# Performance work log

Hardware: AMD Instinct MI355X
Metric: run time of the kernel (lower is better)

## Reference

```python
import jax, jax.numpy as jnp
import numpy as np

B, T, D = 2, 2048, 1024
H = 16
HD = D // H  # 64

def setup_inputs() -> dict:
    key = jax.random.key(0)
    k1, k2, k3 = jax.random.split(key, 3)
    x = jax.random.normal(k1, (B, T, D), dtype=jnp.float32)
    # Linear weights stored as [in, out] for x @ W (torch stores [out, in])
    W_qkv = jax.random.normal(k2, (D, 3 * D), dtype=jnp.float32) * (1.0 / np.sqrt(D))
    W_proj = jax.random.normal(k3, (D, D), dtype=jnp.float32) * (1.0 / np.sqrt(D))
    return {"x": x, "W_qkv": W_qkv, "W_proj": W_proj}

def reference(x, W_qkv, W_proj):
    Bx, Tx, C = x.shape
    qkv = x @ W_qkv                             # [B, T, 3D]
    q, k, v = jnp.split(qkv, 3, axis=-1)        # each [B, T, D]
    # [B, T, H, HD] -> [B, H, T, HD]
    q = q.reshape(Bx, Tx, H, HD).transpose(0, 2, 1, 3)
    k = k.reshape(Bx, Tx, H, HD).transpose(0, 2, 1, 3)
    v = v.reshape(Bx, Tx, H, HD).transpose(0, 2, 1, 3)
    scale = 1.0 / np.sqrt(HD).astype(np.float32)
    att = jnp.einsum('bhqd,bhkd->bhqk', q, k) * scale  # [B, H, T, T]
    causal = jnp.tril(jnp.ones((Tx, Tx), dtype=bool))
    att = jnp.where(causal[None, None, :, :], att, -jnp.inf)
    att = jax.nn.softmax(att, axis=-1)
    y = jnp.einsum('bhqk,bhkd->bhqd', att, v)   # [B, H, T, HD]
    y = y.transpose(0, 2, 1, 3).reshape(Bx, Tx, C)
    return y @ W_proj
```

## Files before the change

kernel.cpp:

```cpp
#include <hip/hip_runtime.h>

typedef __bf16 bf16x8 __attribute__((ext_vector_type(8)));
typedef __bf16 bf16x4 __attribute__((ext_vector_type(4)));
typedef float f32x4 __attribute__((ext_vector_type(4)));
typedef unsigned short u16;
typedef unsigned int u32;
typedef u32 u32x4 __attribute__((ext_vector_type(4)));

__device__ __forceinline__ u16 f2bf(float f) {
  u32 u = __builtin_bit_cast(u32, f);
  u += 0x7fffu + ((u >> 16) & 1u);
  return (u16)(u >> 16);
}

__device__ __forceinline__ u32 cvt_pk_bf16(float lo, float hi) {
  u32 r;
  asm("v_cvt_pk_bf16_f32 %0, %1, %2" : "=v"(r) : "v"(lo), "v"(hi));
  return r;
}

__device__ __forceinline__ float ex2(float x) {
  float r;
  asm("v_exp_f32 %0, %1" : "=v"(r) : "v"(x));
  return r;
}

__device__ __forceinline__ void gl_lds16(const u16* g, u16* l) {
  __builtin_amdgcn_global_load_lds(
      (const __attribute__((address_space(1))) u32*)g,
      (__attribute__((address_space(3))) u32*)l, 16, 0, 0);
}

__device__ __forceinline__ bf16x4 tr16(const u16* p) {
  bf16x4 r;
  auto lp = (const __attribute__((address_space(3))) u16*)p;
  asm volatile("ds_read_b64_tr_b16 %0, %1" : "=&v"(r) : "v"(lp));
  return r;
}

__global__ __launch_bounds__(256) void k_cast(const float* __restrict__ in,
                                              u16* __restrict__ out, int n8) {
  int i = blockIdx.x * 256 + threadIdx.x;
  if (i >= n8) return;
  const float4* p = (const float4*)in + (size_t)i * 2;
  float4 a = p[0], b = p[1];
  u16 r[8] = {f2bf(a.x), f2bf(a.y), f2bf(a.z), f2bf(a.w),
              f2bf(b.x), f2bf(b.y), f2bf(b.z), f2bf(b.w)};
  ((uint4*)out)[i] = *(const uint4*)r;
}

__global__ __launch_bounds__(256) void k_tcast(const float* __restrict__ in,
                                               u16* __restrict__ out, int K, int N) {
  __shared__ float tile[32][33];
  int n0 = blockIdx.x * 32, k0 = blockIdx.y * 32;
  int c = threadIdx.x & 31, r0 = (threadIdx.x >> 5) * 4;
#pragma unroll
  for (int rr = 0; rr < 4; ++rr) {
    int r = r0 + rr;
    tile[r][c] = in[(size_t)(k0 + r) * N + n0 + c];
  }
  __syncthreads();
#pragma unroll
  for (int rr = 0; rr < 4; ++rr) {
    int r = r0 + rr;
    out[(size_t)(n0 + r) * K + k0 + c] = f2bf(tile[c][r]);
  }
}

template <int EPI>
__global__ __launch_bounds__(256) void k_gemm(const u16* __restrict__ A,
                                              const u16* __restrict__ Bt,
                                              u16* __restrict__ Qp, u16* __restrict__ Kp,
                                              u16* __restrict__ Vp, float* __restrict__ Cf,
                                              int K) {
  __shared__ char smem[128 * 136 * 2];
  u16* As = (u16*)smem;
  u16* Bs = (u16*)(smem + 32768 / 2 * 2);
  Bs = (u16*)(smem + 16384);
  u16* Cs = (u16*)smem;
  const int tid = threadIdx.x;
  const int lane = tid & 63, wave = tid >> 6;
  const int l15 = lane & 15, l4 = lane >> 4;
  const int wr = wave >> 1, wc = wave & 1;
  const int tm = blockIdx.y, tn = blockIdx.x;

  int srow[4], scol[4];
#pragma unroll
  for (int i = 0; i < 4; ++i) {
    srow[i] = wave * 32 + i * 8 + (lane >> 3);
    scol[i] = ((lane & 7) ^ (srow[i] & 7)) * 8;
  }

  const f32x4 fz = {0.f, 0.f, 0.f, 0.f};
  f32x4 acc[4][4];
#pragma unroll
  for (int a = 0; a < 4; ++a)
#pragma unroll
    for (int b = 0; b < 4; ++b) acc[a][b] = fz;

  const int nk = K >> 6;
  for (int kt = 0; kt < nk; ++kt) {
#pragma unroll
    for (int i = 0; i < 4; ++i)
      gl_lds16(A + (size_t)(tm * 128 + srow[i]) * K + kt * 64 + scol[i],
               &As[(wave * 4 + i) * 512]);
#pragma unroll
    for (int i = 0; i < 4; ++i)
      gl_lds16(Bt + (size_t)(tn * 128 + srow[i]) * K + kt * 64 + scol[i],
               &Bs[(wave * 4 + i) * 512]);
    __syncthreads();
    bf16x8 af[2][4], bfr[2][4];
#pragma unroll
    for (int s = 0; s < 2; ++s) {
#pragma unroll
      for (int mi = 0; mi < 4; ++mi) {
        int row = wr * 64 + mi * 16 + l15;
        int pch = (s * 4 + l4) ^ (row & 7);
        af[s][mi] = *(const bf16x8*)&As[row * 64 + pch * 8];
      }
#pragma unroll
      for (int ni = 0; ni < 4; ++ni) {
        int row = wc * 64 + ni * 16 + l15;
        int pch = (s * 4 + l4) ^ (row & 7);
        bfr[s][ni] = *(const bf16x8*)&Bs[row * 64 + pch * 8];
      }
    }
    __builtin_amdgcn_s_setprio(1);
#pragma unroll
    for (int s = 0; s < 2; ++s)
#pragma unroll
      for (int mi = 0; mi < 4; ++mi)
#pragma unroll
        for (int ni = 0; ni < 4; ++ni)
          acc[mi][ni] = __builtin_amdgcn_mfma_f32_16x16x32_bf16(af[s][mi], bfr[s][ni],
                                                                acc[mi][ni], 0, 0, 0);
    __builtin_amdgcn_s_setprio(0);
    __syncthreads();
  }

  if (EPI == 0) {
#pragma unroll
    for (int ni = 0; ni < 4; ++ni) {
      int colb = wc * 64 + ni * 16;
      float scl = ((tn * 128 + colb) >> 10) == 0 ? 0.180336880f : 1.0f;
#pragma unroll
      for (int mi = 0; mi < 4; ++mi)
#pragma unroll
        for (int r = 0; r < 4; ++r) {
          int rowb = wr * 64 + mi * 16 + l4 * 4 + r;
          Cs[rowb * 136 + colb + l15] = f2bf(acc[mi][ni][r] * scl);
        }
    }
    __syncthreads();
#pragma unroll
    for (int pass = 0; pass < 8; ++pass) {
      int rowb = pass * 16 + (tid >> 4);
      int colb = (tid & 15) * 8;
      uint4 v = *(const uint4*)&Cs[rowb * 136 + colb];
      int rowg = tm * 128 + rowb;
      int b = rowg >> 11, t = rowg & 2047;
      int gcol = tn * 128 + colb;
      int which = gcol >> 10;
      int d = gcol & 1023;
      int h = d >> 6, hd = d & 63;
      u16* dst = which == 0 ? Qp : (which == 1 ? Kp : Vp);
      *(uint4*)&dst[(size_t)(((b * 16 + h) * 2048 + t) * 64 + hd)] = v;
    }
  } else {
    const int rbase = tm * 128 + wr * 64 + l4 * 4;
    const int cbase = tn * 128 + wc * 64 + l15;
#pragma unroll
    for (int mi = 0; mi < 4; ++mi)
#pragma unroll
      for (int r = 0; r < 4; ++r) {
        int rowg = rbase + mi * 16 + r;
#pragma unroll
        for (int ni = 0; ni < 4; ++ni)
          Cf[(size_t)rowg * 1024 + cbase + ni * 16] = acc[mi][ni][r];
      }
  }
}

__global__ __launch_bounds__(256) void k_attn(const u16* __restrict__ Q,
                                              const u16* __restrict__ K,
                                              const u16* __restrict__ V,
                                              u16* __restrict__ Y) {
  __shared__ u16 Kl[4][64 * 64];
  __shared__ u16 Vtr[4][64 * 64];
  const int tid = threadIdx.x, lane = tid & 63, wave = tid >> 6;
  const int l15 = lane & 15, l4 = lane >> 4;
  const int bh = blockIdx.y;
  const int pp = (blockIdx.x + ((blockIdx.y >> 4) << 3)) & 15;
  const int qtA = 31 - pp, qtB = pp;
  const u16* Qb = Q + (size_t)bh * 2048 * 64;
  const u16* Kb = K + (size_t)bh * 2048 * 64;
  const u16* Vb = V + (size_t)bh * 2048 * 64;
  const int b = bh >> 4, h = bh & 15;
  const f32x4 fz = {0.f, 0.f, 0.f, 0.f};

  const int kk0 = wave * 16 + (lane >> 3);
  const int kk1 = kk0 + 8;
  const int lcol0 = ((lane & 7) ^ (kk0 & 7)) * 8;
  const int lcol1 = ((lane & 7) ^ (kk1 & 7)) * 8;
  int vk[2], vhd[2];
#pragma unroll
  for (int i = 0; i < 2; ++i) {
    int o = (wave * 2 + i) * 512 + lane * 8;
    vk[i] = ((o >> 6) & 15) * 4 + ((o >> 4) & 3);
    vhd[i] = ((o >> 10) << 4) + (o & 8);
  }

  auto stage = [&](int buf, int kt) {
    gl_lds16(Kb + (size_t)(kt * 64 + kk0) * 64 + lcol0, &Kl[buf][(wave * 2 + 0) * 512]);
    gl_lds16(Kb + (size_t)(kt * 64 + kk1) * 64 + lcol1, &Kl[buf][(wave * 2 + 1) * 512]);
    gl_lds16(Vb + (size_t)(kt * 64 + vk[0]) * 64 + vhd[0], &Vtr[buf][(wave * 2 + 0) * 512]);
    gl_lds16(Vb + (size_t)(kt * 64 + vk[1]) * 64 + vhd[1], &Vtr[buf][(wave * 2 + 1) * 512]);
  };

  bf16x8 qfA[2], qfB[2];
  {
    int qrA = qtA * 64 + wave * 16 + l15;
    int qrB = qtB * 64 + wave * 16 + l15;
    qfA[0] = *(const bf16x8*)&Qb[(size_t)qrA * 64 + l4 * 8];
    qfA[1] = *(const bf16x8*)&Qb[(size_t)qrA * 64 + 32 + l4 * 8];
    qfB[0] = *(const bf16x8*)&Qb[(size_t)qrB * 64 + l4 * 8];
    qfB[1] = *(const bf16x8*)&Qb[(size_t)qrB * 64 + 32 + l4 * 8];
  }
  f32x4 oA[4] = {fz, fz, fz, fz}, oB[4] = {fz, fz, fz, fz};
  float mA = -1e30f, lsA = 0.f, mB = -1e30f, lsB = 0.f;

  stage(0, 0);
  stage(1, 1);
  stage(2, 2);

  int cur = 0, kt = 0;

#pragma unroll 1
  for (; kt <= qtB; ++kt) {
    asm volatile("s_waitcnt vmcnt(8)" ::: "memory");
    __builtin_amdgcn_s_barrier();
    __builtin_amdgcn_sched_barrier(0);

    f32x4 sA[4] = {fz, fz, fz, fz}, sB[4] = {fz, fz, fz, fz};
    __builtin_amdgcn_s_setprio(1);
#pragma unroll
    for (int s = 0; s < 2; ++s)
#pragma unroll
      for (int nb = 0; nb < 4; ++nb) {
        int kk = nb * 16 + l15;
        int ch = (s * 4 + l4) ^ (kk & 7);
        bf16x8 kf = *(const bf16x8*)&Kl[cur][kk * 64 + ch * 8];
        sA[nb] = __builtin_amdgcn_mfma_f32_16x16x32_bf16(kf, qfA[s], sA[nb], 0, 0, 0);
        sB[nb] = __builtin_amdgcn_mfma_f32_16x16x32_bf16(kf, qfB[s], sB[nb], 0, 0, 0);
      }
    __builtin_amdgcn_s_setprio(0);

    float vA[16], vB[16];
#pragma unroll
    for (int nb = 0; nb < 4; ++nb)
#pragma unroll
      for (int r = 0; r < 4; ++r) {
        vA[nb * 4 + r] = sA[nb][r];
        vB[nb * 4 + r] = sB[nb][r];
      }
    if (kt == qtB) {
      int qg = wave * 16 + l15;
#pragma unroll
      for (int i = 0; i < 16; ++i) {
        int kg = (i >> 2) * 16 + l4 * 4 + (i & 3);
        if (kg > qg) vB[i] = -1e30f;
      }
    }
    float tA[8], tB[8];
#pragma unroll
    for (int i = 0; i < 8; ++i) {
      tA[i] = fmaxf(vA[2 * i], vA[2 * i + 1]);
      tB[i] = fmaxf(vB[2 * i], vB[2 * i + 1]);
    }
#pragma unroll
    for (int i = 0; i < 4; ++i) {
      tA[i] = fmaxf(tA[i], tA[i + 4]);
      tB[i] = fmaxf(tB[i], tB[i + 4]);
    }
    float mxA = fmaxf(fmaxf(tA[0], tA[2]), fmaxf(tA[1], tA[3]));
    float mxB = fmaxf(fmaxf(tB[0], tB[2]), fmaxf(tB[1], tB[3]));
    if (!__all(fmaxf(mxA - mA, mxB - mB) <= 8.0f)) {
      float mrA = fmaxf(mxA, __shfl_xor(mxA, 16));
      float mrB = fmaxf(mxB, __shfl_xor(mxB, 16));
      mrA = fmaxf(mrA, __shfl_xor(mrA, 32));
      mrB = fmaxf(mrB, __shfl_xor(mrB, 32));
      float mnA = fmaxf(mA, mrA), mnB = fmaxf(mB, mrB);
      float aA = ex2(mA - mnA), aB = ex2(mB - mnB);
      mA = mnA;
      mB = mnB;
      lsA *= aA;
      lsB *= aB;
#pragma unroll
      for (int hb = 0; hb < 4; ++hb)
#pragma unroll
        for (int r = 0; r < 4; ++r) {
          oA[hb][r] *= aA;
          oB[hb][r] *= aB;
        }
    }
    float pA[16], pB[16];
#pragma unroll
    for (int i = 0; i < 16; ++i) {
      pA[i] = ex2(vA[i] - mA);
      pB[i] = ex2(vB[i] - mB);
    }
    float uA[8], uB[8];
#pragma unroll
    for (int i = 0; i < 8; ++i) {
      uA[i] = pA[2 * i] + pA[2 * i + 1];
      uB[i] = pB[2 * i] + pB[2 * i + 1];
    }
#pragma unroll
    for (int i = 0; i < 4; ++i) {
      uA[i] += uA[i + 4];
      uB[i] += uB[i + 4];
    }
    lsA += (uA[0] + uA[2]) + (uA[1] + uA[3]);
    lsB += (uB[0] + uB[2]) + (uB[1] + uB[3]);
    bf16x8 pfA[2], pfB[2];
#pragma unroll
    for (int s = 0; s < 2; ++s) {
      u32x4 wa, wb;
      wa.x = cvt_pk_bf16(pA[8 * s + 0], pA[8 * s + 1]);
      wb.x = cvt_pk_bf16(pB[8 * s + 0], pB[8 * s + 1]);
      wa.y = cvt_pk_bf16(pA[8 * s + 2], pA[8 * s + 3]);
      wb.y = cvt_pk_bf16(pB[8 * s + 2], pB[8 * s + 3]);
      wa.z = cvt_pk_bf16(pA[8 * s + 4], pA[8 * s + 5]);
      wb.z = cvt_pk_bf16(pB[8 * s + 4], pB[8 * s + 5]);
      wa.w = cvt_pk_bf16(pA[8 * s + 6], pA[8 * s + 7]);
      wb.w = cvt_pk_bf16(pB[8 * s + 6], pB[8 * s + 7]);
      pfA[s] = __builtin_bit_cast(bf16x8, wa);
      pfB[s] = __builtin_bit_cast(bf16x8, wb);
    }
    bf16x8 vf[2][4];
#pragma unroll
    for (int s = 0; s < 2; ++s)
#pragma unroll
      for (int hb = 0; hb < 4; ++hb) {
        bf16x4 ta = tr16(&Vtr[cur][(hb * 16 + s * 8) * 64 + lane * 4]);
        bf16x4 tb = tr16(&Vtr[cur][(hb * 16 + s * 8 + 4) * 64 + lane * 4]);
        vf[s][hb] = __builtin_shufflevector(ta, tb, 0, 1, 2, 3, 4, 5, 6, 7);
      }
    asm volatile("s_waitcnt lgkmcnt(0)" ::: "memory");
    __builtin_amdgcn_sched_barrier(0);
    __builtin_amdgcn_s_setprio(1);
#pragma unroll
    for (int s = 0; s < 2; ++s)
#pragma unroll
      for (int hb = 0; hb < 4; ++hb) {
        oA[hb] = __builtin_amdgcn_mfma_f32_16x16x32_bf16(vf[s][hb], pfA[s], oA[hb], 0, 0, 0);
        oB[hb] = __builtin_amdgcn_mfma_f32_16x16x32_bf16(vf[s][hb], pfB[s], oB[hb], 0, 0, 0);
      }
    __builtin_amdgcn_s_setprio(0);

    int nt = kt + 3 > qtA ? qtA : kt + 3;
    stage((cur + 3) & 3, nt);
    cur = (cur + 1) & 3;
  }

#pragma unroll 1
  for (; kt <= qtA; ++kt) {
    asm volatile("s_waitcnt vmcnt(8)" ::: "memory");
    __builtin_amdgcn_s_barrier();
    __builtin_amdgcn_sched_barrier(0);

    f32x4 sA[4] = {fz, fz, fz, fz};
    __builtin_amdgcn_s_setprio(1);
#pragma unroll
    for (int s = 0; s < 2; ++s)
#pragma unroll
      for (int nb = 0; nb < 4; ++nb) {
        int kk = nb * 16 + l15;
        int ch = (s * 4 + l4) ^ (kk & 7);
        bf16x8 kf = *(const bf16x8*)&Kl[cur][kk * 64 + ch * 8];
        sA[nb] = __builtin_amdgcn_mfma_f32_16x16x32_bf16(kf, qfA[s], sA[nb], 0, 0, 0);
      }
    __builtin_amdgcn_s_setprio(0);

    float vA[16];
#pragma unroll
    for (int nb = 0; nb < 4; ++nb)
#pragma unroll
      for (int r = 0; r < 4; ++r) vA[nb * 4 + r] = sA[nb][r];
    if (kt == qtA) {
      int qg = wave * 16 + l15;
#pragma unroll
      for (int i = 0; i < 16; ++i) {
        int kg = (i >> 2) * 16 + l4 * 4 + (i & 3);
        if (kg > qg) vA[i] = -1e30f;
      }
    }
    float tA[8];
#pragma unroll
    for (int i = 0; i < 8; ++i) tA[i] = fmaxf(vA[2 * i], vA[2 * i + 1]);
#pragma unroll
    for (int i = 0; i < 4; ++i) tA[i] = fmaxf(tA[i], tA[i + 4]);
    float mxA = fmaxf(fmaxf(tA[0], tA[2]), fmaxf(tA[1], tA[3]));
    if (!__all(mxA <= mA + 8.0f)) {
      float mrA = fmaxf(mxA, __shfl_xor(mxA, 16));
      mrA = fmaxf(mrA, __shfl_xor(mrA, 32));
      float mnA = fmaxf(mA, mrA);
      float aA = ex2(mA - mnA);
      mA = mnA;
      lsA *= aA;
#pragma unroll
      for (int hb = 0; hb < 4; ++hb)
#pragma unroll
        for (int r = 0; r < 4; ++r) oA[hb][r] *= aA;
    }
    float pA[16];
#pragma unroll
    for (int i = 0; i < 16; ++i) pA[i] = ex2(vA[i] - mA);
    float uA[8];
#pragma unroll
    for (int i = 0; i < 8; ++i) uA[i] = pA[2 * i] + pA[2 * i + 1];
#pragma unroll
    for (int i = 0; i < 4; ++i) uA[i] += uA[i + 4];
    lsA += (uA[0] + uA[2]) + (uA[1] + uA[3]);
    bf16x8 pfA[2];
#pragma unroll
    for (int s = 0; s < 2; ++s) {
      u32x4 wa;
      wa.x = cvt_pk_bf16(pA[8 * s + 0], pA[8 * s + 1]);
      wa.y = cvt_pk_bf16(pA[8 * s + 2], pA[8 * s + 3]);
      wa.z = cvt_pk_bf16(pA[8 * s + 4], pA[8 * s + 5]);
      wa.w = cvt_pk_bf16(pA[8 * s + 6], pA[8 * s + 7]);
      pfA[s] = __builtin_bit_cast(bf16x8, wa);
    }
    bf16x8 vf[2][4];
#pragma unroll
    for (int s = 0; s < 2; ++s)
#pragma unroll
      for (int hb = 0; hb < 4; ++hb) {
        bf16x4 ta = tr16(&Vtr[cur][(hb * 16 + s * 8) * 64 + lane * 4]);
        bf16x4 tb = tr16(&Vtr[cur][(hb * 16 + s * 8 + 4) * 64 + lane * 4]);
        vf[s][hb] = __builtin_shufflevector(ta, tb, 0, 1, 2, 3, 4, 5, 6, 7);
      }
    asm volatile("s_waitcnt lgkmcnt(0)" ::: "memory");
    __builtin_amdgcn_sched_barrier(0);
    __builtin_amdgcn_s_setprio(1);
#pragma unroll
    for (int s = 0; s < 2; ++s)
#pragma unroll
      for (int hb = 0; hb < 4; ++hb)
        oA[hb] = __builtin_amdgcn_mfma_f32_16x16x32_bf16(vf[s][hb], pfA[s], oA[hb], 0, 0, 0);
    __builtin_amdgcn_s_setprio(0);

    int nt = kt + 3 > qtA ? qtA : kt + 3;
    stage((cur + 3) & 3, nt);
    cur = (cur + 1) & 3;
  }

  auto epi = [&](f32x4* accO, float lsum, int qt) {
    float t = lsum + __shfl_xor(lsum, 16);
    t += __shfl_xor(t, 32);
    float inv = 1.0f / t;
    int qg = qt * 64 + wave * 16 + l15;
    u16* yrow = Y + (size_t)(b * 2048 + qg) * 1024 + h * 64;
#pragma unroll
    for (int hb = 0; hb < 4; ++hb) {
      uint2 pk;
      pk.x = cvt_pk_bf16(accO[hb][0] * inv, accO[hb][1] * inv);
      pk.y = cvt_pk_bf16(accO[hb][2] * inv, accO[hb][3] * inv);
      *(uint2*)&yrow[hb * 16 + l4 * 4] = pk;
    }
  };
  epi(oA, lsA, qtA);
  epi(oB, lsB, qtB);
}

extern "C" void kernel_launch(void* const* d_in, const int* in_sizes, int n_in,
                              void* d_out, int out_size, void* d_ws, size_t ws_size,
                              hipStream_t stream) {
  const float* x = (const float*)d_in[0];
  const float* Wqkv = (const float*)d_in[1];
  const float* Wproj = (const float*)d_in[2];
  float* out = (float*)d_out;

  char* ws = (char*)d_ws;
  u16* Xb  = (u16*)(ws + 0);
  u16* Wqt = (u16*)(ws + ((size_t)8 << 20));
  u16* Wpt = (u16*)(ws + ((size_t)14 << 20));
  u16* Qs  = (u16*)(ws + ((size_t)16 << 20));
  u16* Ks  = (u16*)(ws + ((size_t)24 << 20));
  u16* Vs  = (u16*)(ws + ((size_t)32 << 20));
  u16* Yb  = (u16*)(ws + ((size_t)40 << 20));

  k_cast<<<2048, 256, 0, stream>>>(x, Xb, 4096 * 1024 / 8);
  k_tcast<<<dim3(96, 32), 256, 0, stream>>>(Wqkv, Wqt, 1024, 3072);
  k_tcast<<<dim3(32, 32), 256, 0, stream>>>(Wproj, Wpt, 1024, 1024);
  k_gemm<0><<<dim3(24, 32), 256, 0, stream>>>(Xb, Wqt, Qs, Ks, Vs, nullptr, 1024);
  k_attn<<<dim3(16, 32), 256, 0, stream>>>(Qs, Ks, Vs, Yb);
  k_gemm<1><<<dim3(8, 32), 256, 0, stream>>>(Yb, Wpt, nullptr, nullptr, nullptr, out, 1024);
}
```

Measured before the change: 109.9 us.

## Process two KV tiles per iteration in single-query-tile attention tail

After the paired-query phase, the tail loop now restages four KV buffers and processes two key tiles per iteration with a joint online-softmax rescale, halving barrier and max-reduction overhead. The diagonal tile is handled separately with masking. The PV MFMAs are also split per k-half so V transposed loads for one half overlap with the other, lowering register pressure. This adds a barrier and restaging at the phase boundary, and the joint max check may trigger rescales more often.

```diff
diff --git a/kernel.cpp b/kernel.cpp
--- a/kernel.cpp
+++ b/kernel.cpp
@@ -75,8 +75,7 @@
                                               int K) {
   __shared__ char smem[128 * 136 * 2];
   u16* As = (u16*)smem;
-  u16* Bs = (u16*)(smem + 32768 / 2 * 2);
-  Bs = (u16*)(smem + 16384);
+  u16* Bs = (u16*)(smem + 16384);
   u16* Cs = (u16*)smem;
   const int tid = threadIdx.x;
   const int lane = tid & 63, wave = tid >> 6;
@@ -217,6 +216,37 @@
     gl_lds16(Vb + (size_t)(kt * 64 + vk[1]) * 64 + vhd[1], &Vtr[buf][(wave * 2 + 1) * 512]);
   };
 
+  auto qk = [&](int buf, const bf16x8* qf, f32x4* accS) {
+#pragma unroll
+    for (int s = 0; s < 2; ++s)
+#pragma unroll
+      for (int nb = 0; nb < 4; ++nb) {
+        int kk = nb * 16 + l15;
+        int ch = (s * 4 + l4) ^ (kk & 7);
+        bf16x8 kf = *(const bf16x8*)&Kl[buf][kk * 64 + ch * 8];
+        accS[nb] = __builtin_amdgcn_mfma_f32_16x16x32_bf16(kf, qf[s], accS[nb], 0, 0, 0);
+      }
+  };
+  auto pv = [&](int buf, const bf16x8* pf, f32x4* accO) {
+#pragma unroll
+    for (int s = 0; s < 2; ++s) {
+      bf16x8 vf[4];
+#pragma unroll
+      for (int hb = 0; hb < 4; ++hb) {
+        bf16x4 ta = tr16(&Vtr[buf][(hb * 16 + s * 8) * 64 + lane * 4]);
+        bf16x4 tb = tr16(&Vtr[buf][(hb * 16 + s * 8 + 4) * 64 + lane * 4]);
+        vf[hb] = __builtin_shufflevector(ta, tb, 0, 1, 2, 3, 4, 5, 6, 7);
+      }
+      asm volatile("s_waitcnt lgkmcnt(0)" ::: "memory");
+      __builtin_amdgcn_sched_barrier(0);
+      __builtin_amdgcn_s_setprio(1);
+#pragma unroll
+      for (int hb = 0; hb < 4; ++hb)
+        accO[hb] = __builtin_amdgcn_mfma_f32_16x16x32_bf16(vf[hb], pf[s], accO[hb], 0, 0, 0);
+      __builtin_amdgcn_s_setprio(0);
+    }
+  };
+
   bf16x8 qfA[2], qfB[2];
   {
     int qrA = qtA * 64 + wave * 16 + l15;
@@ -232,11 +262,9 @@
   stage(0, 0);
   stage(1, 1);
   stage(2, 2);
-
-  int cur = 0, kt = 0;
-
+  int cur = 0;
 #pragma unroll 1
-  for (; kt <= qtB; ++kt) {
+  for (int kt = 0; kt <= qtB; ++kt) {
     asm volatile("s_waitcnt vmcnt(8)" ::: "memory");
     __builtin_amdgcn_s_barrier();
     __builtin_amdgcn_sched_barrier(0);
@@ -337,63 +365,153 @@
       pfA[s] = __builtin_bit_cast(bf16x8, wa);
       pfB[s] = __builtin_bit_cast(bf16x8, wb);
     }
-    bf16x8 vf[2][4];
-#pragma unroll
-    for (int s = 0; s < 2; ++s)
+#pragma unroll
+    for (int s = 0; s < 2; ++s) {
+      bf16x8 vf[4];
 #pragma unroll
       for (int hb = 0; hb < 4; ++hb) {
         bf16x4 ta = tr16(&Vtr[cur][(hb * 16 + s * 8) * 64 + lane * 4]);
         bf16x4 tb = tr16(&Vtr[cur][(hb * 16 + s * 8 + 4) * 64 + lane * 4]);
-        vf[s][hb] = __builtin_shufflevector(ta, tb, 0, 1, 2, 3, 4, 5, 6, 7);
-      }
-    asm volatile("s_waitcnt lgkmcnt(0)" ::: "memory");
-    __builtin_amdgcn_sched_barrier(0);
-    __builtin_amdgcn_s_setprio(1);
-#pragma unroll
-    for (int s = 0; s < 2; ++s)
+        vf[hb] = __builtin_shufflevector(ta, tb, 0, 1, 2, 3, 4, 5, 6, 7);
+      }
+      asm volatile("s_waitcnt lgkmcnt(0)" ::: "memory");
+      __builtin_amdgcn_sched_barrier(0);
+      __builtin_amdgcn_s_setprio(1);
 #pragma unroll
       for (int hb = 0; hb < 4; ++hb) {
-        oA[hb] = __builtin_amdgcn_mfma_f32_16x16x32_bf16(vf[s][hb], pfA[s], oA[hb], 0, 0, 0);
-        oB[hb] = __builtin_amdgcn_mfma_f32_16x16x32_bf16(vf[s][hb], pfB[s], oB[hb], 0, 0, 0);
-      }
-    __builtin_amdgcn_s_setprio(0);
-
-    int nt = kt + 3 > qtA ? qtA : kt + 3;
+        oA[hb] = __builtin_amdgcn_mfma_f32_16x16x32_bf16(vf[hb], pfA[s], oA[hb], 0, 0, 0);
+        oB[hb] = __builtin_amdgcn_mfma_f32_16x16x32_bf16(vf[hb], pfB[s], oB[hb], 0, 0, 0);
+      }
+      __builtin_amdgcn_s_setprio(0);
+    }
+
+    int nt = kt + 3 > qtB ? qtB : kt + 3;
     stage((cur + 3) & 3, nt);
     cur = (cur + 1) & 3;
   }
 
+  const int t0 = qtB + 1;
+  const int rem = qtA - qtB;
+  const int nd = (rem - 1) >> 1;
+  __builtin_amdgcn_s_barrier();
+  __builtin_amdgcn_sched_barrier(0);
+#pragma unroll
+  for (int i = 0; i < 4; ++i) {
+    int tt = t0 + i > qtA ? qtA : t0 + i;
+    stage(i, tt);
+  }
+
+  auto smx2 = [&](f32x4* s1, f32x4* s2, bf16x8* pf1, bf16x8* pf2) {
+    float v1[16], v2[16];
+#pragma unroll
+    for (int nb = 0; nb < 4; ++nb)
+#pragma unroll
+      for (int r = 0; r < 4; ++r) {
+        v1[nb * 4 + r] = s1[nb][r];
+        v2[nb * 4 + r] = s2[nb][r];
+      }
+    float t1[8], t2[8];
+#pragma unroll
+    for (int i = 0; i < 8; ++i) {
+      t1[i] = fmaxf(v1[2 * i], v1[2 * i + 1]);
+      t2[i] = fmaxf(v2[2 * i], v2[2 * i + 1]);
+    }
+#pragma unroll
+    for (int i = 0; i < 4; ++i) {
+      t1[i] = fmaxf(t1[i], t1[i + 4]);
+      t2[i] = fmaxf(t2[i], t2[i + 4]);
+    }
+    float mx = fmaxf(fmaxf(fmaxf(t1[0], t1[2]), fmaxf(t1[1], t1[3])),
+                     fmaxf(fmaxf(t2[0], t2[2]), fmaxf(t2[1], t2[3])));
+    if (!__all(mx <= mA + 8.0f)) {
+      float mr = fmaxf(mx, __shfl_xor(mx, 16));
+      mr = fmaxf(mr, __shfl_xor(mr, 32));
+      float mn = fmaxf(mA, mr);
+      float a = ex2(mA - mn);
+      mA = mn;
+      lsA *= a;
+#pragma unroll
+      for (int hb = 0; hb < 4; ++hb)
+#pragma unroll
+        for (int r = 0; r < 4; ++r) oA[hb][r] *= a;
+    }
+    float p1[16], p2[16];
+#pragma unroll
+    for (int i = 0; i < 16; ++i) {
+      p1[i] = ex2(v1[i] - mA);
+      p2[i] = ex2(v2[i] - mA);
+    }
+    float u1[8], u2[8];
+#pragma unroll
+    for (int i = 0; i < 8; ++i) {
+      u1[i] = p1[2 * i] + p1[2 * i + 1];
+      u2[i] = p2[2 * i] + p2[2 * i + 1];
+    }
+#pragma unroll
+    for (int i = 0; i < 4; ++i) {
+      u1[i] += u1[i + 4];
+      u2[i] += u2[i + 4];
+    }
+    lsA += (u1[0] + u1[2]) + (u1[1] + u1[3]) + (u2[0] + u2[2]) + (u2[1] + u2[3]);
+#pragma unroll
+    for (int s = 0; s < 2; ++s) {
+      u32x4 w1, w2;
+      w1.x = cvt_pk_bf16(p1[8 * s + 0], p1[8 * s + 1]);
+      w2.x = cvt_pk_bf16(p2[8 * s + 0], p2[8 * s + 1]);
+      w1.y = cvt_pk_bf16(p1[8 * s + 2], p1[8 * s + 3]);
+      w2.y = cvt_pk_bf16(p2[8 * s + 2], p2[8 * s + 3]);
+      w1.z = cvt_pk_bf16(p1[8 * s + 4], p1[8 * s + 5]);
+      w2.z = cvt_pk_bf16(p2[8 * s + 4], p2[8 * s + 5]);
+      w1.w = cvt_pk_bf16(p1[8 * s + 6], p1[8 * s + 7]);
+      w2.w = cvt_pk_bf16(p2[8 * s + 6], p2[8 * s + 7]);
+      pf1[s] = __builtin_bit_cast(bf16x8, w1);
+      pf2[s] = __builtin_bit_cast(bf16x8, w2);
+    }
+  };
+
 #pragma unroll 1
-  for (; kt <= qtA; ++kt) {
+  for (int j = 0; j < nd; ++j) {
     asm volatile("s_waitcnt vmcnt(8)" ::: "memory");
     __builtin_amdgcn_s_barrier();
     __builtin_amdgcn_sched_barrier(0);
-
+    int b0 = (2 * j) & 3, b1 = (2 * j + 1) & 3;
+
+    f32x4 s1[4] = {fz, fz, fz, fz}, s2[4] = {fz, fz, fz, fz};
+    __builtin_amdgcn_s_setprio(1);
+    qk(b0, qfA, s1);
+    qk(b1, qfA, s2);
+    __builtin_amdgcn_s_setprio(0);
+    bf16x8 pf1[2], pf2[2];
+    smx2(s1, s2, pf1, pf2);
+    pv(b0, pf1, oA);
+    pv(b1, pf2, oA);
+
+    __builtin_amdgcn_s_barrier();
+    __builtin_amdgcn_sched_barrier(0);
+    int ta = t0 + 2 * j + 4, tb2 = t0 + 2 * j + 5;
+    stage(b0, ta > qtA ? qtA : ta);
+    stage(b1, tb2 > qtA ? qtA : tb2);
+  }
+
+  {
+    asm volatile("s_waitcnt vmcnt(8)" ::: "memory");
+    __builtin_amdgcn_s_barrier();
+    __builtin_amdgcn_sched_barrier(0);
+    int buf = (rem - 1) & 3;
     f32x4 sA[4] = {fz, fz, fz, fz};
     __builtin_amdgcn_s_setprio(1);
-#pragma unroll
-    for (int s = 0; s < 2; ++s)
-#pragma unroll
-      for (int nb = 0; nb < 4; ++nb) {
-        int kk = nb * 16 + l15;
-        int ch = (s * 4 + l4) ^ (kk & 7);
-        bf16x8 kf = *(const bf16x8*)&Kl[cur][kk * 64 + ch * 8];
-        sA[nb] = __builtin_amdgcn_mfma_f32_16x16x32_bf16(kf, qfA[s], sA[nb], 0, 0, 0);
-      }
+    qk(buf, qfA, sA);
     __builtin_amdgcn_s_setprio(0);
-
     float vA[16];
 #pragma unroll
     for (int nb = 0; nb < 4; ++nb)
 #pragma unroll
       for (int r = 0; r < 4; ++r) vA[nb * 4 + r] = sA[nb][r];
-    if (kt == qtA) {
-      int qg = wave * 16 + l15;
-#pragma unroll
-      for (int i = 0; i < 16; ++i) {
-        int kg = (i >> 2) * 16 + l4 * 4 + (i & 3);
-        if (kg > qg) vA[i] = -1e30f;
-      }
+    int qg = wave * 16 + l15;
+#pragma unroll
+    for (int i = 0; i < 16; ++i) {
+      int kg = (i >> 2) * 16 + l4 * 4 + (i & 3);
+      if (kg > qg) vA[i] = -1e30f;
     }
     float tA[8];
 #pragma unroll
@@ -432,28 +550,7 @@
       wa.w = cvt_pk_bf16(pA[8 * s + 6], pA[8 * s + 7]);
       pfA[s] = __builtin_bit_cast(bf16x8, wa);
     }
-    bf16x8 vf[2][4];
-#pragma unroll
-    for (int s = 0; s < 2; ++s)
-#pragma unroll
-      for (int hb = 0; hb < 4; ++hb) {
-        bf16x4 ta = tr16(&Vtr[cur][(hb * 16 + s * 8) * 64 + lane * 4]);
-        bf16x4 tb = tr16(&Vtr[cur][(hb * 16 + s * 8 + 4) * 64 + lane * 4]);
-        vf[s][hb] = __builtin_shufflevector(ta, tb, 0, 1, 2, 3, 4, 5, 6, 7);
-      }
-    asm volatile("s_waitcnt lgkmcnt(0)" ::: "memory");
-    __builtin_amdgcn_sched_barrier(0);
-    __builtin_amdgcn_s_setprio(1);
-#pragma unroll
-    for (int s = 0; s < 2; ++s)
-#pragma unroll
-      for (int hb = 0; hb < 4; ++hb)
-        oA[hb] = __builtin_amdgcn_mfma_f32_16x16x32_bf16(vf[s][hb], pfA[s], oA[hb], 0, 0, 0);
-    __builtin_amdgcn_s_setprio(0);
-
-    int nt = kt + 3 > qtA ? qtA : kt + 3;
-    stage((cur + 3) & 3, nt);
-    cur = (cur + 1) & 3;
+    pv(buf, pfA, oA);
   }
 
   auto epi = [&](f32x4* accO, float lsum, int qt) {
```

Result: faster. 106.8 us (-2.8%).
